# Optimization experiments

Hardware: AMD Instinct MI355X
Metric: run time of the kernel (lower is better)

## Reference

```python
import jax, jax.numpy as jnp
import numpy as np
import math

IN_FEATURES = 512
KERNEL = 3
EPS = 1e-08
GAIN = 1.0 / math.sqrt(IN_FEATURES * KERNEL * KERNEL)  # lr_multiplier=1


def setup_inputs() -> dict:
    key = jax.random.key(0)
    k1, k2, k3 = jax.random.split(key, 3)
    x = jax.random.normal(k1, (16, 512, 32, 32), dtype=jnp.float32)
    style = jax.random.normal(k2, (16, 512), dtype=jnp.float32)
    weight = jax.random.normal(k3, (512, 512, 3, 3), dtype=jnp.float32)
    return {"x": x, "style": style, "weight": weight}


def reference(x, style, weight):
    # w: [B, O, I, k, k] = gain-scaled weight modulated per-sample by style over input channels
    w = (weight * GAIN)[None] * style[:, None, :, None, None]
    # demodulate: rsqrt of sum of squares over (I, kh, kw) per (B, O)
    sigma = jax.lax.rsqrt(jnp.sum(jnp.square(w), axis=(2, 3, 4)) + EPS)
    w = w * sigma[:, :, None, None, None]
    # per-sample conv2d with padding='same' (stride 1, k=3 -> pad 1)
    def conv_one(xi, wi):  # xi: [C,H,W], wi: [O,I,k,k]
        return jax.lax.conv_general_dilated(
            xi[None], wi, window_strides=(1, 1), padding='SAME',
            dimension_numbers=('NCHW', 'OIHW', 'NCHW'))[0]
    return jax.vmap(conv_one)(x, w)  # [B, O, H, W]
```

## Files before the change

kernel.cpp:

```cpp
#include <hip/hip_runtime.h>
#include <hip/hip_bf16.h>

#define EPSF 1e-8f
#define GAINF 0.014731391274719739f

typedef __attribute__((ext_vector_type(8))) __bf16 bf16x8;
typedef __attribute__((ext_vector_type(4))) __bf16 bf16x4;
typedef __attribute__((ext_vector_type(16))) float f32x16;

#define GLOAD_LDS16(gp, lp) __builtin_amdgcn_global_load_lds( \
    (const __attribute__((address_space(1))) unsigned int*)(gp), \
    (__attribute__((address_space(3))) unsigned int*)(lp), 16, 0, 0)

__global__ void k_prep(const float* __restrict__ x, const float* __restrict__ style,
                       const float* __restrict__ w, float* __restrict__ S,
                       __hip_bfloat16* __restrict__ wbf, __hip_bfloat16* __restrict__ xs) {
  int blk = blockIdx.x, tid = threadIdx.x;
  if (blk < 2048) {
    __shared__ float tile[64][65];
    int b = blk >> 7, rem = blk & 127, ct = rem >> 4, pt = rem & 15;
    int p0 = pt * 64, c0 = ct * 64;
    int tx = tid & 63, ty = tid >> 6;
#pragma unroll
    for (int k = 0; k < 16; ++k) {
      int ci = ty + k * 4;
      tile[ci][tx] = x[((b * 512) + (c0 + ci)) * 1024 + p0 + tx];
    }
    __syncthreads();
    int tq = tid & 15, py = tid >> 4;
    int c = c0 + tq * 4;
    int cb = c >> 5, cw = c & 31;
    float st0 = style[b * 512 + c], st1 = style[b * 512 + c + 1];
    float st2 = style[b * 512 + c + 2], st3 = style[b * 512 + c + 3];
#pragma unroll
    for (int k = 0; k < 4; ++k) {
      int pl = py + k * 16;
      int p = p0 + pl;
      int y = p >> 5, xx = p & 31;
      int site = (y + 1) * 34 + (xx + 1);
      bf16x4 v;
      v[0] = (__bf16)(tile[tq * 4 + 0][pl] * st0);
      v[1] = (__bf16)(tile[tq * 4 + 1][pl] * st1);
      v[2] = (__bf16)(tile[tq * 4 + 2][pl] * st2);
      v[3] = (__bf16)(tile[tq * 4 + 3][pl] * st3);
      *reinterpret_cast<bf16x4*>(xs + (size_t)(((b * 16 + cb) * 1156 + site) * 32 + cw)) = v;
    }
  } else if (blk < 3072) {
    int idx = (blk - 2048) * 256 + tid;
    int o = idx >> 9, i = idx & 511;
    const float* p = w + (size_t)idx * 9;
    float s = 0.f;
#pragma unroll
    for (int t = 0; t < 9; ++t) {
      float v = p[t];
      s += v * v;
      wbf[(size_t)t * 262144 + (i >> 5) * 16384 + o * 32 + (i & 31)] = __float2bfloat16(v);
    }
    S[idx] = s;
  } else {
    int bb = blk - 3072;
    int b = bb >> 4, cb = bb & 15;
    for (int i2 = tid; i2 < 528; i2 += 256) {
      int sb = i2 >> 2, q = i2 & 3;
      int yp, xp;
      if (sb < 34) { yp = 0; xp = sb; }
      else if (sb < 68) { yp = 33; xp = sb - 34; }
      else { int t2 = sb - 68; yp = 1 + (t2 >> 1); xp = (t2 & 1) * 33; }
      float4 z = {0.f, 0.f, 0.f, 0.f};
      *reinterpret_cast<float4*>(xs + (size_t)(((b * 16 + cb) * 1156 + yp * 34 + xp) * 32 + q * 8)) = z;
    }
  }
}

__global__ void k_sigma(const float* __restrict__ style, const float* __restrict__ S,
                        float* __restrict__ esc) {
  __shared__ float s2[8192];
  __shared__ float red[4][16];
  int tid = threadIdx.x, o = blockIdx.x;
  for (int idx = tid; idx < 8192; idx += 256) {
    float v = style[idx];
    s2[idx] = v * v;
  }
  __syncthreads();
  float acc[16];
#pragma unroll
  for (int b = 0; b < 16; ++b) acc[b] = 0.f;
  for (int i = tid; i < 512; i += 256) {
    float s = S[o * 512 + i];
#pragma unroll
    for (int b = 0; b < 16; ++b) acc[b] += s2[b * 512 + i] * s;
  }
#pragma unroll
  for (int b = 0; b < 16; ++b)
#pragma unroll
    for (int off = 32; off; off >>= 1) acc[b] += __shfl_down(acc[b], off);
  int lane = tid & 63, wv = tid >> 6;
  if (lane == 0)
#pragma unroll
    for (int b = 0; b < 16; ++b) red[wv][b] = acc[b];
  __syncthreads();
  if (tid < 16) {
    float s = red[0][tid] + red[1][tid] + red[2][tid] + red[3][tid];
    esc[tid * 512 + o] = GAINF * rsqrtf(s * (GAINF * GAINF) + EPSF);
  }
}

__global__ __launch_bounds__(64, 1) void k_conv(
    const __hip_bfloat16* __restrict__ wbf, const __hip_bfloat16* __restrict__ xs,
    const float* __restrict__ esc, float* __restrict__ out) {
  __shared__ __hip_bfloat16 ldsB[2 * 6528];
  int g = blockIdx.x;
  int xcd = g & 7, sblk = g >> 3;
  int m = sblk >> 4;
  int n = xcd * 16 + (sblk & 15);
  int b = n >> 3, nt = n & 7;
  int row0 = nt * 4;
  int lane = threadIdx.x;
  int l31 = lane & 31, lhi = lane >> 5;

  int roff[13];
#pragma unroll
  for (int j = 0; j < 13; ++j) {
    int idx = lane + j * 64;
    int site = idx >> 2, q0 = idx & 3;
    int qs = q0 ^ ((site >> 1) & 3);
    roff[j] = site * 32 + qs * 8;
  }

#define STAGE(cbv) do { \
    const __hip_bfloat16* _g = xs + (size_t)((b * 16 + (cbv)) * 1156 + row0 * 34) * 32; \
    __hip_bfloat16* _l = ldsB + ((cbv) & 1) * 6528 + lane * 8; \
    _Pragma("unroll") \
    for (int _j = 0; _j < 12; ++_j) GLOAD_LDS16(_g + roff[_j], _l + _j * 512); \
    if (lane < 48) GLOAD_LDS16(_g + roff[12], _l + 12 * 512); \
  } while (0)

  int wrow = (m * 64 + l31) * 32 + lhi * 8;
#define LOADA(dst, t_, cb_) do { \
    const __hip_bfloat16* _p = wbf + (size_t)(t_) * 262144 + (cb_) * 16384 + wrow; \
    dst[0][0] = *reinterpret_cast<const bf16x8*>(_p); \
    dst[0][1] = *reinterpret_cast<const bf16x8*>(_p + 1024); \
    dst[1][0] = *reinterpret_cast<const bf16x8*>(_p + 16); \
    dst[1][1] = *reinterpret_cast<const bf16x8*>(_p + 1024 + 16); \
  } while (0)

  f32x16 acc[2][4];
#pragma unroll
  for (int i = 0; i < 2; ++i)
#pragma unroll
    for (int j = 0; j < 4; ++j)
#pragma unroll
      for (int e = 0; e < 16; ++e) acc[i][j][e] = 0.f;

  bf16x8 aC[2][2], aN[2][2];
  STAGE(0);
  LOADA(aC, 0, 0);

  for (int cb = 0; cb < 16; ++cb) {
    __syncthreads();
    if (cb < 15) STAGE(cb + 1);
    const __hip_bfloat16* lb = ldsB + (cb & 1) * 6528;
#pragma unroll
    for (int t = 0; t < 9; ++t) {
      const int dy = t / 3, dx = t - dy * 3;
      if (cb < 15 || t < 8) {
        int tn = (t == 8) ? 0 : t + 1;
        int cbn = (t == 8) ? cb + 1 : cb;
        LOADA(aN, tn, cbn);
      }
      int s[4], sw[4];
#pragma unroll
      for (int ns = 0; ns < 4; ++ns) {
        s[ns] = (ns + dy) * 34 + l31 + dx;
        sw[ns] = (s[ns] >> 1) & 3;
      }
#pragma unroll
      for (int k2 = 0; k2 < 2; ++k2) {
        int ko = (k2 << 1) | lhi;
        bf16x8 bf[4];
#pragma unroll
        for (int ns = 0; ns < 4; ++ns)
          bf[ns] = *reinterpret_cast<const bf16x8*>(&lb[(s[ns] * 4 + (ko ^ sw[ns])) * 8]);
#pragma unroll
        for (int ns = 0; ns < 4; ++ns) {
          acc[0][ns] = __builtin_amdgcn_mfma_f32_32x32x16_bf16(aC[k2][0], bf[ns], acc[0][ns], 0, 0, 0);
          acc[1][ns] = __builtin_amdgcn_mfma_f32_32x32x16_bf16(aC[k2][1], bf[ns], acc[1][ns], 0, 0, 0);
        }
      }
#pragma unroll
      for (int k2 = 0; k2 < 2; ++k2)
#pragma unroll
        for (int ms = 0; ms < 2; ++ms)
          aC[k2][ms] = aN[k2][ms];
    }
  }
  int pxb = nt * 128 + l31;
#pragma unroll
  for (int ms = 0; ms < 2; ++ms)
#pragma unroll
    for (int reg = 0; reg < 16; ++reg) {
      int o = m * 64 + ms * 32 + (reg & 3) + ((reg >> 2) << 3) + (lhi << 2);
      float e = esc[(b << 9) + o];
#pragma unroll
      for (int ns = 0; ns < 4; ++ns)
        out[(size_t)((b << 9) + o) * 1024 + pxb + ns * 32] = acc[ms][ns][reg] * e;
    }
#undef STAGE
#undef LOADA
}

extern "C" void kernel_launch(void* const* d_in, const int* in_sizes, int n_in,
                              void* d_out, int out_size, void* d_ws, size_t ws_size,
                              hipStream_t stream) {
  const float* x = (const float*)d_in[0];
  const float* style = (const float*)d_in[1];
  const float* w = (const float*)d_in[2];
  float* out = (float*)d_out;
  char* ws = (char*)d_ws;
  __hip_bfloat16* wbf = (__hip_bfloat16*)(ws);
  __hip_bfloat16* xs  = (__hip_bfloat16*)(ws + 4718592);
  float* S   = (float*)(ws + 23658496);
  float* esc = (float*)(ws + 24707072);

  hipLaunchKernelGGL(k_prep, dim3(3328), dim3(256), 0, stream, x, style, w, S, wbf, xs);
  hipLaunchKernelGGL(k_sigma, dim3(512), dim3(256), 0, stream, style, S, esc);
  hipLaunchKernelGGL(k_conv, dim3(1024), dim3(64), 0, stream, wbf, xs, esc, out);
}
```

Before: 174.1 us.

## Double conv output-channel tile, drop barrier, and restructure input prep transpose

The conv kernel now computes 128 output channels per block instead of 64, with a 4x4 MFMA accumulator grid, and the grid shrinks to 512 blocks. This halves how often the same input slab is staged per output and reuses each B fragment across more MFMAs. The per-iteration __syncthreads is replaced by explicit s_waitcnt vmcnt waits, which is possible because each block is a single wave. The prep kernel is rewritten to use float4 input loads, a swizzled LDS transpose and 16-byte packed bf16 stores, with the halo zeroing merged into the same blocks. The trade-off is heavier register and accumulator pressure and only two single-wave blocks per CU, which makes latency hiding harder.

```diff
diff --git a/kernel.cpp b/kernel.cpp
--- a/kernel.cpp
+++ b/kernel.cpp
@@ -5,48 +5,73 @@
 #define GAINF 0.014731391274719739f
 
 typedef __attribute__((ext_vector_type(8))) __bf16 bf16x8;
-typedef __attribute__((ext_vector_type(4))) __bf16 bf16x4;
 typedef __attribute__((ext_vector_type(16))) float f32x16;
 
 #define GLOAD_LDS16(gp, lp) __builtin_amdgcn_global_load_lds( \
     (const __attribute__((address_space(1))) unsigned int*)(gp), \
     (__attribute__((address_space(3))) unsigned int*)(lp), 16, 0, 0)
+
+static __device__ __forceinline__ unsigned pkbf(float a, float b) {
+  unsigned ua = __bfloat16_as_ushort(__float2bfloat16(a));
+  unsigned ub = __bfloat16_as_ushort(__float2bfloat16(b));
+  return ua | (ub << 16);
+}
 
 __global__ void k_prep(const float* __restrict__ x, const float* __restrict__ style,
                        const float* __restrict__ w, float* __restrict__ S,
                        __hip_bfloat16* __restrict__ wbf, __hip_bfloat16* __restrict__ xs) {
   int blk = blockIdx.x, tid = threadIdx.x;
-  if (blk < 2048) {
-    __shared__ float tile[64][65];
-    int b = blk >> 7, rem = blk & 127, ct = rem >> 4, pt = rem & 15;
-    int p0 = pt * 64, c0 = ct * 64;
-    int tx = tid & 63, ty = tid >> 6;
-#pragma unroll
-    for (int k = 0; k < 16; ++k) {
-      int ci = ty + k * 4;
-      tile[ci][tx] = x[((b * 512) + (c0 + ci)) * 1024 + p0 + tx];
+  if (blk < 1024) {
+    __shared__ float lt[256 * 33];
+    int b = blk >> 6, cb = (blk >> 2) & 15, q = blk & 3;
+    int c = tid >> 3, i8 = tid & 7;
+    float st = style[b * 512 + cb * 32 + c];
+    const float4* xp = reinterpret_cast<const float4*>(
+        x + ((size_t)(b * 512 + cb * 32 + c) * 1024 + q * 256 + i8 * 32));
+    float4 v[8];
+#pragma unroll
+    for (int j = 0; j < 8; ++j) v[j] = xp[j];
+    int swz = (c + 4 * i8) & 31;
+#pragma unroll
+    for (int j = 0; j < 8; ++j) {
+      int p = i8 * 32 + j * 4;
+      lt[(p + 0) * 33 + swz] = v[j].x * st;
+      lt[(p + 1) * 33 + swz] = v[j].y * st;
+      lt[(p + 2) * 33 + swz] = v[j].z * st;
+      lt[(p + 3) * 33 + swz] = v[j].w * st;
     }
     __syncthreads();
-    int tq = tid & 15, py = tid >> 4;
-    int c = c0 + tq * 4;
-    int cb = c >> 5, cw = c & 31;
-    float st0 = style[b * 512 + c], st1 = style[b * 512 + c + 1];
-    float st2 = style[b * 512 + c + 2], st3 = style[b * 512 + c + 3];
+    int p = tid;
+    int pq = q * 256 + p;
+    int y = pq >> 5, xx = pq & 31;
+    int site = (y + 1) * 34 + (xx + 1);
+    __hip_bfloat16* dst = xs + ((size_t)(b * 16 + cb) * 1156 + site) * 32;
+    int rs = 4 * (p >> 5);
 #pragma unroll
     for (int k = 0; k < 4; ++k) {
-      int pl = py + k * 16;
-      int p = p0 + pl;
-      int y = p >> 5, xx = p & 31;
-      int site = (y + 1) * 34 + (xx + 1);
-      bf16x4 v;
-      v[0] = (__bf16)(tile[tq * 4 + 0][pl] * st0);
-      v[1] = (__bf16)(tile[tq * 4 + 1][pl] * st1);
-      v[2] = (__bf16)(tile[tq * 4 + 2][pl] * st2);
-      v[3] = (__bf16)(tile[tq * 4 + 3][pl] * st3);
-      *reinterpret_cast<bf16x4*>(xs + (size_t)(((b * 16 + cb) * 1156 + site) * 32 + cw)) = v;
-    }
-  } else if (blk < 3072) {
-    int idx = (blk - 2048) * 256 + tid;
+      uint4 ov;
+      ov.x = pkbf(lt[p * 33 + ((8 * k + 0 + rs) & 31)], lt[p * 33 + ((8 * k + 1 + rs) & 31)]);
+      ov.y = pkbf(lt[p * 33 + ((8 * k + 2 + rs) & 31)], lt[p * 33 + ((8 * k + 3 + rs) & 31)]);
+      ov.z = pkbf(lt[p * 33 + ((8 * k + 4 + rs) & 31)], lt[p * 33 + ((8 * k + 5 + rs) & 31)]);
+      ov.w = pkbf(lt[p * 33 + ((8 * k + 6 + rs) & 31)], lt[p * 33 + ((8 * k + 7 + rs) & 31)]);
+      reinterpret_cast<uint4*>(dst)[k] = ov;
+    }
+    if (tid < 33) {
+      int sbi = q * 33 + tid;
+      if (sbi < 132) {
+        int yp, xp2;
+        if (sbi < 34) { yp = 0; xp2 = sbi; }
+        else if (sbi < 68) { yp = 33; xp2 = sbi - 34; }
+        else { int t2 = sbi - 68; yp = 1 + (t2 >> 1); xp2 = (t2 & 1) * 33; }
+        uint4 z = {0u, 0u, 0u, 0u};
+        uint4* zp = reinterpret_cast<uint4*>(
+            xs + ((size_t)(b * 16 + cb) * 1156 + yp * 34 + xp2) * 32);
+#pragma unroll
+        for (int k = 0; k < 4; ++k) zp[k] = z;
+      }
+    }
+  } else {
+    int idx = (blk - 1024) * 256 + tid;
     int o = idx >> 9, i = idx & 511;
     const float* p = w + (size_t)idx * 9;
     float s = 0.f;
@@ -54,21 +79,9 @@
     for (int t = 0; t < 9; ++t) {
       float v = p[t];
       s += v * v;
-      wbf[(size_t)t * 262144 + (i >> 5) * 16384 + o * 32 + (i & 31)] = __float2bfloat16(v);
+      wbf[(size_t)(t * 16 + (i >> 5)) * 16384 + o * 32 + (i & 31)] = __float2bfloat16(v);
     }
     S[idx] = s;
-  } else {
-    int bb = blk - 3072;
-    int b = bb >> 4, cb = bb & 15;
-    for (int i2 = tid; i2 < 528; i2 += 256) {
-      int sb = i2 >> 2, q = i2 & 3;
-      int yp, xp;
-      if (sb < 34) { yp = 0; xp = sb; }
-      else if (sb < 68) { yp = 33; xp = sb - 34; }
-      else { int t2 = sb - 68; yp = 1 + (t2 >> 1); xp = (t2 & 1) * 33; }
-      float4 z = {0.f, 0.f, 0.f, 0.f};
-      *reinterpret_cast<float4*>(xs + (size_t)(((b * 16 + cb) * 1156 + yp * 34 + xp) * 32 + q * 8)) = z;
-    }
   }
 }
 
@@ -110,9 +123,9 @@
     const float* __restrict__ esc, float* __restrict__ out) {
   __shared__ __hip_bfloat16 ldsB[2 * 6528];
   int g = blockIdx.x;
-  int xcd = g & 7, sblk = g >> 3;
-  int m = sblk >> 4;
-  int n = xcd * 16 + (sblk & 15);
+  int xcd = g & 7, sb = g >> 3;
+  int m = sb >> 4;
+  int n = xcd * 16 + (sb & 15);
   int b = n >> 3, nt = n & 7;
   int row0 = nt * 4;
   int lane = threadIdx.x;
@@ -126,40 +139,46 @@
     int qs = q0 ^ ((site >> 1) & 3);
     roff[j] = site * 32 + qs * 8;
   }
+  const size_t slab = ((size_t)(b * 16) * 1156 + row0 * 34) * 32;
 
 #define STAGE(cbv) do { \
-    const __hip_bfloat16* _g = xs + (size_t)((b * 16 + (cbv)) * 1156 + row0 * 34) * 32; \
+    const __hip_bfloat16* _g = xs + slab + (size_t)(cbv) * (1156 * 32); \
     __hip_bfloat16* _l = ldsB + ((cbv) & 1) * 6528 + lane * 8; \
     _Pragma("unroll") \
     for (int _j = 0; _j < 12; ++_j) GLOAD_LDS16(_g + roff[_j], _l + _j * 512); \
     if (lane < 48) GLOAD_LDS16(_g + roff[12], _l + 12 * 512); \
   } while (0)
 
-  int wrow = (m * 64 + l31) * 32 + lhi * 8;
+  const __hip_bfloat16* wlane = wbf + (m * 128 + l31) * 32 + lhi * 8;
 #define LOADA(dst, t_, cb_) do { \
-    const __hip_bfloat16* _p = wbf + (size_t)(t_) * 262144 + (cb_) * 16384 + wrow; \
-    dst[0][0] = *reinterpret_cast<const bf16x8*>(_p); \
-    dst[0][1] = *reinterpret_cast<const bf16x8*>(_p + 1024); \
-    dst[1][0] = *reinterpret_cast<const bf16x8*>(_p + 16); \
-    dst[1][1] = *reinterpret_cast<const bf16x8*>(_p + 1024 + 16); \
+    const __hip_bfloat16* _p = wlane + (size_t)((t_) * 16 + (cb_)) * 16384; \
+    _Pragma("unroll") \
+    for (int _ms = 0; _ms < 4; ++_ms) { \
+      dst[0][_ms] = *reinterpret_cast<const bf16x8*>(_p + _ms * 1024); \
+      dst[1][_ms] = *reinterpret_cast<const bf16x8*>(_p + _ms * 1024 + 16); \
+    } \
   } while (0)
 
-  f32x16 acc[2][4];
-#pragma unroll
-  for (int i = 0; i < 2; ++i)
+  f32x16 acc[4][4];
+#pragma unroll
+  for (int i = 0; i < 4; ++i)
 #pragma unroll
     for (int j = 0; j < 4; ++j)
 #pragma unroll
       for (int e = 0; e < 16; ++e) acc[i][j][e] = 0.f;
 
-  bf16x8 aC[2][2], aN[2][2];
+  bf16x8 aC[2][4], aN[2][4];
   STAGE(0);
   LOADA(aC, 0, 0);
 
   for (int cb = 0; cb < 16; ++cb) {
-    __syncthreads();
-    if (cb < 15) STAGE(cb + 1);
-    const __hip_bfloat16* lb = ldsB + (cb & 1) * 6528;
+    if (cb < 15) {
+      STAGE(cb + 1);
+      asm volatile("s_waitcnt vmcnt(21)" ::: "memory");
+    } else {
+      asm volatile("s_waitcnt vmcnt(8)" ::: "memory");
+    }
+    const __hip_bfloat16* B = ldsB + (cb & 1) * 6528;
 #pragma unroll
     for (int t = 0; t < 9; ++t) {
       const int dy = t / 3, dx = t - dy * 3;
@@ -168,42 +187,40 @@
         int cbn = (t == 8) ? cb + 1 : cb;
         LOADA(aN, tn, cbn);
       }
-      int s[4], sw[4];
-#pragma unroll
-      for (int ns = 0; ns < 4; ++ns) {
-        s[ns] = (ns + dy) * 34 + l31 + dx;
-        sw[ns] = (s[ns] >> 1) & 3;
-      }
 #pragma unroll
       for (int k2 = 0; k2 < 2; ++k2) {
         int ko = (k2 << 1) | lhi;
-        bf16x8 bf[4];
+        bf16x8 bfr[4];
+#pragma unroll
+        for (int ns = 0; ns < 4; ++ns) {
+          int s = (ns + dy) * 34 + l31 + dx;
+          bfr[ns] = *reinterpret_cast<const bf16x8*>(&B[(s * 4 + (ko ^ ((s >> 1) & 3))) * 8]);
+        }
 #pragma unroll
         for (int ns = 0; ns < 4; ++ns)
-          bf[ns] = *reinterpret_cast<const bf16x8*>(&lb[(s[ns] * 4 + (ko ^ sw[ns])) * 8]);
-#pragma unroll
-        for (int ns = 0; ns < 4; ++ns) {
-          acc[0][ns] = __builtin_amdgcn_mfma_f32_32x32x16_bf16(aC[k2][0], bf[ns], acc[0][ns], 0, 0, 0);
-          acc[1][ns] = __builtin_amdgcn_mfma_f32_32x32x16_bf16(aC[k2][1], bf[ns], acc[1][ns], 0, 0, 0);
-        }
+#pragma unroll
+          for (int ms = 0; ms < 4; ++ms)
+            acc[ms][ns] = __builtin_amdgcn_mfma_f32_32x32x16_bf16(aC[k2][ms], bfr[ns],
+                                                                  acc[ms][ns], 0, 0, 0);
       }
 #pragma unroll
       for (int k2 = 0; k2 < 2; ++k2)
 #pragma unroll
-        for (int ms = 0; ms < 2; ++ms)
+        for (int ms = 0; ms < 4; ++ms)
           aC[k2][ms] = aN[k2][ms];
     }
   }
   int pxb = nt * 128 + l31;
 #pragma unroll
-  for (int ms = 0; ms < 2; ++ms)
+  for (int ms = 0; ms < 4; ++ms)
 #pragma unroll
     for (int reg = 0; reg < 16; ++reg) {
-      int o = m * 64 + ms * 32 + (reg & 3) + ((reg >> 2) << 3) + (lhi << 2);
+      int o = m * 128 + ms * 32 + (reg & 3) + ((reg >> 2) << 3) + (lhi << 2);
       float e = esc[(b << 9) + o];
+      float* op = out + ((size_t)((b << 9) + o) << 10) + pxb;
 #pragma unroll
       for (int ns = 0; ns < 4; ++ns)
-        out[(size_t)((b << 9) + o) * 1024 + pxb + ns * 32] = acc[ms][ns][reg] * e;
+        op[ns * 32] = acc[ms][ns][reg] * e;
     }
 #undef STAGE
 #undef LOADA
@@ -222,7 +239,7 @@
   float* S   = (float*)(ws + 23658496);
   float* esc = (float*)(ws + 24707072);
 
-  hipLaunchKernelGGL(k_prep, dim3(3328), dim3(256), 0, stream, x, style, w, S, wbf, xs);
+  hipLaunchKernelGGL(k_prep, dim3(2048), dim3(256), 0, stream, x, style, w, S, wbf, xs);
   hipLaunchKernelGGL(k_sigma, dim3(512), dim3(256), 0, stream, style, S, esc);
-  hipLaunchKernelGGL(k_conv, dim3(1024), dim3(64), 0, stream, wbf, xs, esc, out);
-}
+  hipLaunchKernelGGL(k_conv, dim3(512), dim3(64), 0, stream, wbf, xs, esc, out);
+}
```

Measured after the change: 316.2 us. 1.82x slower.
